# Kernel tuning notes

Hardware: AMD Instinct MI355X
Metric: run time of the kernel (lower is better)

## Reference

```python
import jax, jax.numpy as jnp
import numpy as np

NS, NW, E, DIN, OUT, H = 100_000, 400_000, 500_000, 64, 64, 4


def setup_inputs() -> dict:
    key = jax.random.key(0)
    ks = jax.random.split(key, 26)
    s = 1.0 / np.sqrt(DIN)
    sg = 1.0 / np.sqrt(OUT)
    inp = {
        "x_sites": jax.random.normal(ks[0], (NS, DIN), jnp.float32),
        "x_wells": jax.random.normal(ks[1], (NW, DIN), jnp.float32),
        "edge_sw_src": jax.random.randint(ks[2], (E,), 0, NS, jnp.int32),
        "edge_sw_dst": jax.random.randint(ks[3], (E,), 0, NW, jnp.int32),
        "edge_ws_src": jax.random.randint(ks[4], (E,), 0, NW, jnp.int32),
        "edge_ws_dst": jax.random.randint(ks[5], (E,), 0, NS, jnp.int32),
        # GAT ('pfas_sites','distance','gw_wells'), heads=4, concat=False
        "W_sw": jax.random.normal(ks[6], (DIN, H * OUT), jnp.float32) * s,
        "att_src_sw": jax.random.normal(ks[7], (H, OUT), jnp.float32) * sg,
        "att_dst_sw": jax.random.normal(ks[8], (H, OUT), jnp.float32) * sg,
        "b_sw": jnp.zeros((OUT,), jnp.float32),
        # SAGE ('gw_wells','distance','pfas_sites')
        "Wl_ws": jax.random.normal(ks[9], (DIN, OUT), jnp.float32) * s,
        "bl_ws": jnp.zeros((OUT,), jnp.float32),
        "Wr_ws": jax.random.normal(ks[10], (DIN, OUT), jnp.float32) * s,
        # GAT ('pfas_sites','self_loop','pfas_sites'), add_self_loops=True -> identity edges
        "W_ss": jax.random.normal(ks[11], (DIN, H * OUT), jnp.float32) * s,
        "att_src_ss": jax.random.normal(ks[12], (H, OUT), jnp.float32) * sg,
        "att_dst_ss": jax.random.normal(ks[13], (H, OUT), jnp.float32) * sg,
        "b_ss": jnp.zeros((OUT,), jnp.float32),
        # SAGE ('gw_wells','self_loop','gw_wells') with identity edges
        "Wl_ww": jax.random.normal(ks[14], (DIN, OUT), jnp.float32) * s,
        "bl_ww": jnp.zeros((OUT,), jnp.float32),
        "Wr_ww": jax.random.normal(ks[15], (DIN, OUT), jnp.float32) * s,
        # output heads
        "Wg": jax.random.normal(ks[16], (OUT, 1), jnp.float32) * sg,
        "bg": jnp.zeros((1,), jnp.float32),
        "Wsit": jax.random.normal(ks[17], (OUT, 1), jnp.float32) * sg,
        "bsit": jnp.zeros((1,), jnp.float32),
    }
    return inp


def _gat(x_src, x_dst, src, dst, W, a_src, a_dst, b, n_dst):
    """PyG GATConv, concat=False (mean over heads), negative_slope=0.2."""
    h, c = a_src.shape
    xs = (x_src @ W).reshape(-1, h, c)  # [Ns,H,C]
    xd = (x_dst @ W).reshape(-1, h, c)  # [Nd,H,C]
    al_s = jnp.einsum("nhc,hc->nh", xs, a_src)
    al_d = jnp.einsum("nhc,hc->nh", xd, a_dst)
    e = jax.nn.leaky_relu(al_s[src] + al_d[dst], 0.2)  # [E,H]
    m = jax.ops.segment_max(e, dst, num_segments=n_dst)
    ex = jnp.exp(e - m[dst])
    denom = jax.ops.segment_sum(ex, dst, num_segments=n_dst)
    alpha = ex / denom[dst]  # edge-softmax per dst node
    msg = xs[src] * alpha[:, :, None]  # [E,H,C] dominant intermediate
    out = jax.ops.segment_sum(msg, dst, num_segments=n_dst)
    return out.mean(axis=1) + b


def _sage(x_src, x_dst, src, dst, Wl, bl, Wr, n_dst):
    """PyG SAGEConv, mean aggregation, root_weight=True."""
    ssum = jax.ops.segment_sum(x_src[src], dst, num_segments=n_dst)
    cnt = jax.ops.segment_sum(jnp.ones((src.shape[0],), x_src.dtype), dst, num_segments=n_dst)
    mean = ssum / jnp.maximum(cnt, 1.0)[:, None]  # empty neighborhood -> 0 (PyG mean scatter)
    return mean @ Wl + bl + x_dst @ Wr


def reference(x_sites, x_wells, edge_sw_src, edge_sw_dst, edge_ws_src, edge_ws_dst,
              W_sw, att_src_sw, att_dst_sw, b_sw, Wl_ws, bl_ws, Wr_ws,
              W_ss, att_src_ss, att_dst_ss, b_ss, Wl_ww, bl_ww, Wr_ww,
              Wg, bg, Wsit, bsit):
    # relation 1: GAT sites -> wells
    gw = _gat(x_sites, x_wells, edge_sw_src, edge_sw_dst, W_sw, att_src_sw, att_dst_sw, b_sw, NW)
    # relation 4: SAGE self-loop on wells; identity edges -> mean == x itself
    gw = gw + (x_wells @ Wl_ww + bl_ww + x_wells @ Wr_ww)  # HeteroConv aggr='sum'
    # relation 2: SAGE wells -> sites
    si = _sage(x_wells, x_sites, edge_ws_src, edge_ws_dst, Wl_ws, bl_ws, Wr_ws, NS)
    # relation 3: GAT self-loop on sites (add_self_loops=True -> identity edge set);
    # softmax over a single self edge is 1, so output = mean over heads of lin(x) + bias
    si = si + (x_sites @ W_ss).reshape(NS, H, OUT).mean(axis=1) + b_ss
    # post: relu -> dropout (eval mode: identity) -> linear -> leaky_relu(0.01)
    gw = jax.nn.relu(gw)
    si = jax.nn.relu(si)
    o_gw = jax.nn.leaky_relu(gw @ Wg + bg, 0.01)   # [NW, 1]
    o_si = jax.nn.leaky_relu(si @ Wsit + bsit, 0.01)  # [NS, 1]
    return o_gw, o_si
```

## Files before the change

kernel.cpp:

```cpp
#include <hip/hip_runtime.h>

#define NS_ 100000
#define NW_ 400000
#define NE_ 500000
#define EPB 2048

#define SP_BLKS  ((NS_ + 63) / 64)
#define HG_BLKS  ((NE_ + 255) / 256)
#define SAGE_BLKS (NS_ / 16)
#define GAT_BLKS  (NW_ / 16)

typedef float f32x4_t __attribute__((ext_vector_type(4)));
typedef unsigned u32x4_t __attribute__((ext_vector_type(4)));

__device__ __forceinline__ float lrelu02(float x) { return x > 0.f ? x : 0.2f * x; }
__device__ __forceinline__ float bf2f(unsigned short u) {
    return __uint_as_float(((unsigned)u) << 16);
}
__device__ __forceinline__ unsigned short f2bf(float f) {
    unsigned u = __float_as_uint(f);
    u += 0x7FFFu + ((u >> 16) & 1u);
    return (unsigned short)(u >> 16);
}
__device__ __forceinline__ unsigned pk(float lo, float hi) {
    return (unsigned)f2bf(lo) | ((unsigned)f2bf(hi) << 16);
}
__device__ __forceinline__ void mfma_bf16(f32x4_t& acc, u32x4_t a, u32x4_t b) {
    asm volatile("v_mfma_f32_16x16x32_bf16 %0, %1, %2, %0" : "+v"(acc) : "v"(a), "v"(b));
}

__global__ void __launch_bounds__(256)
k_prep(const float* __restrict__ W_sw, const float* __restrict__ att_src,
       const float* __restrict__ att_dst,
       const float* __restrict__ Wl_ww, const float* __restrict__ Wr_ww,
       const float* __restrict__ Wl_ws, const float* __restrict__ Wr_ws,
       const float* __restrict__ W_ss,
       float* __restrict__ vd, float* __restrict__ vs,
       u32x4_t* __restrict__ fw, u32x4_t* __restrict__ fs,
       u32x4_t* __restrict__ fsp)
{
    const int tid = threadIdx.x;
    {
        int d = tid >> 2, h = tid & 3;
        const float4* wp = (const float4*)(W_sw + d * 256 + h * 64);
        const float4* ad = (const float4*)(att_dst + h * 64);
        const float4* as = (const float4*)(att_src + h * 64);
        float accd = 0.f, accs = 0.f;
#pragma unroll
        for (int c = 0; c < 16; ++c) {
            float4 wv = wp[c]; float4 dv = ad[c]; float4 sv = as[c];
            accd += wv.x * dv.x + wv.y * dv.y + wv.z * dv.z + wv.w * dv.w;
            accs += wv.x * sv.x + wv.y * sv.y + wv.z * sv.z + wv.w * sv.w;
        }
        vd[d * 4 + h] = accd;
        vs[d * 4 + h] = accs;
    }
    for (int idx = tid; idx < 512; idx += 256) {
        int f = idx >> 6, lane = idx & 63;
        int kc = f >> 2, ct = f & 3, q = lane >> 4, n = lane & 15;
        int c = ct * 16 + n;
        u32x4_t d;
#pragma unroll
        for (int i = 0; i < 4; ++i) {
            int k = kc * 32 + q * 8 + 2 * i;
            d[i] = pk(Wl_ww[k * 64 + c] + Wr_ww[k * 64 + c],
                      Wl_ww[(k + 1) * 64 + c] + Wr_ww[(k + 1) * 64 + c]);
        }
        fw[idx] = d;
    }
    for (int idx = tid; idx < 1024; idx += 256) {
        int f = idx >> 6, lane = idx & 63;
        int kc = f >> 2, ct = f & 3, q = lane >> 4, n = lane & 15;
        int c = ct * 16 + n;
        u32x4_t d;
#pragma unroll
        for (int i = 0; i < 4; ++i) {
            int k = kc * 32 + q * 8 + 2 * i;
            float lo, hi;
            if (k < 64) {
                lo = Wl_ws[k * 64 + c];
                hi = Wl_ws[(k + 1) * 64 + c];
            } else {
                int kk = k - 64;
                lo = Wr_ws[kk * 64 + c] + 0.25f * (W_ss[kk * 256 + c] + W_ss[kk * 256 + 64 + c] +
                                                   W_ss[kk * 256 + 128 + c] + W_ss[kk * 256 + 192 + c]);
                hi = Wr_ws[(kk + 1) * 64 + c] + 0.25f * (W_ss[(kk + 1) * 256 + c] + W_ss[(kk + 1) * 256 + 64 + c] +
                                                         W_ss[(kk + 1) * 256 + 128 + c] + W_ss[(kk + 1) * 256 + 192 + c]);
            }
            d[i] = pk(lo, hi);
        }
        fs[idx] = d;
    }
    for (int idx = tid; idx < 2048; idx += 256) {
        int f = idx >> 6, lane = idx & 63;
        int kc = f >> 4, ct = f & 15, q = lane >> 4, n = lane & 15;
        int c = ct * 16 + n;
        u32x4_t d;
#pragma unroll
        for (int i = 0; i < 4; ++i) {
            int k = kc * 32 + q * 8 + 2 * i;
            d[i] = pk(W_sw[k * 256 + c], W_sw[(k + 1) * 256 + c]);
        }
        fsp[idx] = d;
    }
}

#define SP_PAD 264
__global__ void __launch_bounds__(256)
k_main1(const float* __restrict__ x_sites, const u32x4_t* __restrict__ fsp,
        const float* __restrict__ vs, unsigned short* __restrict__ xs,
        float* __restrict__ al_s,
        const int* __restrict__ d1, int* __restrict__ h1,
        const int* __restrict__ d2, int* __restrict__ h2)
{
    __shared__ float smem1[8704];
    const int tid = threadIdx.x;
    const int bid = blockIdx.x;
    if (bid >= SP_BLKS) {
        int hb = bid - SP_BLKS;
        int rel = hb / HG_BLKS;
        int e = (hb % HG_BLKS) * 256 + tid;
        if (e < NE_) {
            if (rel == 0) atomicAdd(&h1[d1[e]], 1);
            else          atomicAdd(&h2[d2[e]], 1);
        }
        return;
    }
    unsigned short* stg = (unsigned short*)smem1;
    float* vsl = smem1 + 8448 / 2 * 0 + 8448;
    vsl = smem1 + 8448;
    vsl[tid] = vs[tid];
    __syncthreads();
    const int wave = __builtin_amdgcn_readfirstlane(tid >> 6);
    const int lane = tid & 63, q = lane >> 4, n = lane & 15;
    const int sbase = bid * 64 + wave * 16;
    const int srow = min(sbase + n, NS_ - 1);
    const float* xr = x_sites + (size_t)srow * 64 + q * 8;
    float4 x0 = *(const float4*)(xr);
    float4 x1 = *(const float4*)(xr + 4);
    float4 x2 = *(const float4*)(xr + 32);
    float4 x3 = *(const float4*)(xr + 36);
    u32x4_t am0 = { pk(x0.x, x0.y), pk(x0.z, x0.w), pk(x1.x, x1.y), pk(x1.z, x1.w) };
    u32x4_t am1 = { pk(x2.x, x2.y), pk(x2.z, x2.w), pk(x3.x, x3.y), pk(x3.z, x3.w) };
    float pa[4];
#pragma unroll
    for (int h = 0; h < 4; ++h) {
        const float* v0 = &vsl[(q * 8) * 4 + h];
        const float* v1 = &vsl[(32 + q * 8) * 4 + h];
        pa[h] = x0.x * v0[0]  + x0.y * v0[4]  + x0.z * v0[8]  + x0.w * v0[12]
              + x1.x * v0[16] + x1.y * v0[20] + x1.z * v0[24] + x1.w * v0[28]
              + x2.x * v1[0]  + x2.y * v1[4]  + x2.z * v1[8]  + x2.w * v1[12]
              + x3.x * v1[16] + x3.y * v1[20] + x3.z * v1[24] + x3.w * v1[28];
    }
#pragma unroll
    for (int h = 0; h < 4; ++h) {
        pa[h] += __shfl_xor(pa[h], 16, 64);
        pa[h] += __shfl_xor(pa[h], 32, 64);
    }
    if (q == 0 && sbase + n < NS_)
        *(float4*)(al_s + (size_t)(sbase + n) * 4) = make_float4(pa[0], pa[1], pa[2], pa[3]);

    f32x4_t acc[16];
#pragma unroll
    for (int ct = 0; ct < 16; ++ct) acc[ct] = (f32x4_t){0, 0, 0, 0};
    asm volatile("s_nop 3" : "+v"(am0), "+v"(am1));
#pragma unroll
    for (int ct = 0; ct < 16; ++ct) mfma_bf16(acc[ct], am0, fsp[ct * 64 + lane]);
#pragma unroll
    for (int ct = 0; ct < 16; ++ct) mfma_bf16(acc[ct], am1, fsp[(16 + ct) * 64 + lane]);
    asm volatile("s_nop 7\n\ts_nop 7" ::: "memory");
    unsigned short* ss = stg + wave * (16 * SP_PAD);
#pragma unroll
    for (int ct = 0; ct < 16; ++ct)
#pragma unroll
        for (int reg = 0; reg < 4; ++reg)
            ss[(q * 4 + reg) * SP_PAD + ct * 16 + n] = f2bf(acc[ct][reg]);
    __builtin_amdgcn_s_waitcnt(0);
#pragma unroll
    for (int i = 0; i < 8; ++i) {
        int g = i * 64 + lane;
        int r = g >> 5, c = g & 31;
        if (sbase + r < NS_) {
            u32x4_t v = *(const u32x4_t*)(ss + r * SP_PAD + c * 8);
            *(u32x4_t*)(xs + (size_t)(sbase + r) * 256 + c * 8) = v;
        }
    }
}

__global__ void __launch_bounds__(256)
k_scan1_2(const int* __restrict__ h1, int n1, int* __restrict__ b1, int nb1,
          const int* __restrict__ h2, int n2, int* __restrict__ b2)
{
    __shared__ int red[256];
    const int tid = threadIdx.x;
    const int bx = blockIdx.x;
    const int* hist; int n; int* bsum; int blk;
    if (bx < nb1) { hist = h1; n = n1; bsum = b1; blk = bx; }
    else          { hist = h2; n = n2; bsum = b2; blk = bx - nb1; }
    int base = blk * EPB + tid * 8;
    int s = 0;
#pragma unroll
    for (int i = 0; i < 8; ++i) { int idx = base + i; if (idx < n) s += hist[idx]; }
    red[tid] = s;
    __syncthreads();
    for (int off = 128; off > 0; off >>= 1) {
        if (tid < off) red[tid] += red[tid + off];
        __syncthreads();
    }
    if (tid == 0) bsum[blk] = red[0];
}

__global__ void __launch_bounds__(256)
k_scan2_2(int* __restrict__ b1, int nb1, int* __restrict__ b2, int nb2)
{
    __shared__ int sh[256];
    const int tid = threadIdx.x;
    int* bsum = blockIdx.x == 0 ? b1 : b2;
    int nb = blockIdx.x == 0 ? nb1 : nb2;
    sh[tid] = (tid < nb) ? bsum[tid] : 0;
    __syncthreads();
    for (int off = 1; off < 256; off <<= 1) {
        int u = (tid >= off) ? sh[tid - off] : 0;
        __syncthreads();
        sh[tid] += u;
        __syncthreads();
    }
    if (tid < nb) bsum[tid] = (tid == 0) ? 0 : sh[tid - 1];
}

__global__ void __launch_bounds__(256)
k_scan3_2(const int* __restrict__ h1, int n1, const int* __restrict__ b1,
          int* __restrict__ rp1, int* __restrict__ cu1, int nb1,
          const int* __restrict__ h2, int n2, const int* __restrict__ b2,
          int* __restrict__ rp2, int* __restrict__ cu2)
{
    __shared__ int tsum[256];
    const int tid = threadIdx.x;
    const int bx = blockIdx.x;
    const int* hist; int n; const int* bsum; int* rowptr; int* cursor; int blk;
    if (bx < nb1) { hist = h1; n = n1; bsum = b1; rowptr = rp1; cursor = cu1; blk = bx; }
    else          { hist = h2; n = n2; bsum = b2; rowptr = rp2; cursor = cu2; blk = bx - nb1; }
    int base = blk * EPB + tid * 8;
    int v[8]; int s = 0;
#pragma unroll
    for (int i = 0; i < 8; ++i) {
        int idx = base + i;
        v[i] = (idx < n) ? hist[idx] : 0;
        s += v[i];
    }
    tsum[tid] = s;
    __syncthreads();
    for (int off = 1; off < 256; off <<= 1) {
        int u = (tid >= off) ? tsum[tid - off] : 0;
        __syncthreads();
        tsum[tid] += u;
        __syncthreads();
    }
    int texcl = tsum[tid] - s;
    int run = bsum[blk] + texcl;
#pragma unroll
    for (int i = 0; i < 8; ++i) {
        int idx = base + i;
        if (idx < n) { rowptr[idx] = run; cursor[idx] = run; run += v[i]; }
    }
    if (blk == 0 && tid == 0) rowptr[n] = NE_;
}

__global__ void __launch_bounds__(256)
k_scatter2(const int* __restrict__ s1, const int* __restrict__ d1,
           int* __restrict__ c1, int* __restrict__ o1,
           const int* __restrict__ s2, const int* __restrict__ d2,
           int* __restrict__ c2, int* __restrict__ o2)
{
    int e = blockIdx.x * 256 + threadIdx.x;
    if (e >= NE_) return;
    if (blockIdx.y == 0) { int p = atomicAdd(&c1[d1[e]], 1); o1[p] = s1[e]; }
    else                 { int p = atomicAdd(&c2[d2[e]], 1); o2[p] = s2[e]; }
}

__global__ void __launch_bounds__(256)
k_main6(const float* __restrict__ x_sites, const float* __restrict__ x_wells,
        const int* __restrict__ rp_ws, const int* __restrict__ csr_ws,
        const u32x4_t* __restrict__ fs, const float* __restrict__ bl_ws,
        const float* __restrict__ b_ss, const float* __restrict__ Wsit,
        const float* __restrict__ bsit,
        const float* __restrict__ vd, const int* __restrict__ rp_sw,
        const int* __restrict__ csr_sw, const float* __restrict__ al_s,
        const unsigned short* __restrict__ xs, const float* __restrict__ b_sw,
        const float* __restrict__ bl_ww, const u32x4_t* __restrict__ fw,
        const float* __restrict__ Wg, const float* __restrict__ bg,
        float* __restrict__ out)
{
    __shared__ float smem[2400];
    const int tid = threadIdx.x;
    const int bid = blockIdx.x;

    if (bid < SAGE_BLKS) {
        unsigned* mnB = (unsigned*)smem;
        unsigned* xB  = (unsigned*)(smem + 576);
        float* dl     = smem + 1152;
        float* biasl  = smem + 2240;
        float* wsl    = smem + 2304;
        float* res    = smem + 2368;
        if (tid < 64) { biasl[tid] = bl_ws[tid] + b_ss[tid]; wsl[tid] = Wsit[tid]; }
        const int sl = tid >> 4, p = tid & 15;
        const int s = bid * 16 + sl;
        const int r0 = rp_ws[s], r1 = rp_ws[s + 1];
        float4 m4 = {0.f, 0.f, 0.f, 0.f};
        for (int j = r0; j < r1; ++j) {
            int wsrc = csr_ws[j];
            float4 xv = ((const float4*)(x_wells + (size_t)wsrc * 64))[p];
            m4.x += xv.x; m4.y += xv.y; m4.z += xv.z; m4.w += xv.w;
        }
        if (r1 > r0) {
            float rc = 1.f / (float)(r1 - r0);
            m4.x *= rc; m4.y *= rc; m4.z *= rc; m4.w *= rc;
        }
        {
            int c0 = (2 * p + 8 * sl) & 31;
            mnB[sl * 36 + c0]     = pk(m4.x, m4.y);
            mnB[sl * 36 + c0 + 1] = pk(m4.z, m4.w);
            float4 xv = *(const float4*)(x_sites + (size_t)s * 64 + 4 * p);
            xB[sl * 36 + c0]     = pk(xv.x, xv.y);
            xB[sl * 36 + c0 + 1] = pk(xv.z, xv.w);
        }
        __syncthreads();
        const int wave = __builtin_amdgcn_readfirstlane(tid >> 6);
        const int lane = tid & 63, q = lane >> 4, n = lane & 15;
        const int b0 = (4 * q + 8 * n) & 31;
        const int b1 = (16 + 4 * q + 8 * n) & 31;
        u32x4_t am0 = *(const u32x4_t*)&mnB[n * 36 + b0];
        u32x4_t am1 = *(const u32x4_t*)&mnB[n * 36 + b1];
        u32x4_t ax0 = *(const u32x4_t*)&xB[n * 36 + b0];
        u32x4_t ax1 = *(const u32x4_t*)&xB[n * 36 + b1];
        f32x4_t acc = {0, 0, 0, 0};
        asm volatile("s_nop 3" : "+v"(am0), "+v"(am1), "+v"(ax0), "+v"(ax1), "+v"(acc));
        mfma_bf16(acc, am0, fs[wave * 64 + lane]);
        mfma_bf16(acc, am1, fs[(4 + wave) * 64 + lane]);
        mfma_bf16(acc, ax0, fs[(8 + wave) * 64 + lane]);
        mfma_bf16(acc, ax1, fs[(12 + wave) * 64 + lane]);
        asm volatile("s_nop 7\n\ts_nop 7" : "+v"(acc));
#pragma unroll
        for (int reg = 0; reg < 4; ++reg)
            dl[(q * 4 + reg) * 68 + wave * 16 + n] = acc[reg];
        __syncthreads();
        const int c0 = 4 * p;
        float4 dv = *(const float4*)&dl[sl * 68 + c0];
        float t0 = dv.x + biasl[c0];
        float t1 = dv.y + biasl[c0 + 1];
        float t2 = dv.z + biasl[c0 + 2];
        float t3 = dv.w + biasl[c0 + 3];
        float pr = fmaxf(t0, 0.f) * wsl[c0] + fmaxf(t1, 0.f) * wsl[c0 + 1] +
                   fmaxf(t2, 0.f) * wsl[c0 + 2] + fmaxf(t3, 0.f) * wsl[c0 + 3];
        pr += __shfl_xor(pr, 1, 64);
        pr += __shfl_xor(pr, 2, 64);
        pr += __shfl_xor(pr, 4, 64);
        pr += __shfl_xor(pr, 8, 64);
        if (p == 0) res[sl] = pr + bsit[0];
        __syncthreads();
        if (tid < 16) {
            float v = res[tid];
            out[(size_t)NW_ + bid * 16 + tid] = v > 0.f ? v : 0.01f * v;
        }
        return;
    }

    {
        const int gb = bid - SAGE_BLKS;
        float* vdl    = smem;
        unsigned* xwB = (unsigned*)(smem + 272);
        float* dl     = smem + 848;
        float* biasl  = smem + 1936;
        float* wgl    = smem + 2000;
        float* res    = smem + 2064;
        vdl[(tid >> 4) * 17 + (tid & 15)] = vd[tid];
        if (tid < 64) { biasl[tid] = b_sw[tid] + bl_ww[tid]; wgl[tid] = Wg[tid]; }
        __syncthreads();
        const int wl = tid >> 4, p = tid & 15;
        const int w = gb * 16 + wl;
        const int r0 = rp_sw[w], r1 = rp_sw[w + 1];
        float h0, h1, h2, h3;
        {
            float4 xv = *(const float4*)(x_wells + (size_t)w * 64 + 4 * p);
            int c0 = (2 * p + 8 * wl) & 31;
            xwB[wl * 36 + c0]     = pk(xv.x, xv.y);
            xwB[wl * 36 + c0 + 1] = pk(xv.z, xv.w);
            const float* vp = &vdl[p * 17];
            h0 = xv.x * vp[0] + xv.y * vp[4] + xv.z * vp[8]  + xv.w * vp[12];
            h1 = xv.x * vp[1] + xv.y * vp[5] + xv.z * vp[9]  + xv.w * vp[13];
            h2 = xv.x * vp[2] + xv.y * vp[6] + xv.z * vp[10] + xv.w * vp[14];
            h3 = xv.x * vp[3] + xv.y * vp[7] + xv.z * vp[11] + xv.w * vp[15];
        }
#pragma unroll
        for (int off = 1; off < 16; off <<= 1) {
            h0 += __shfl_xor(h0, off, 64);
            h1 += __shfl_xor(h1, off, 64);
            h2 += __shfl_xor(h2, off, 64);
            h3 += __shfl_xor(h3, off, 64);
        }
        float den0 = 0, den1 = 0, den2 = 0, den3 = 0;
        float n0[4] = {0, 0, 0, 0}, n1[4] = {0, 0, 0, 0};
        float n2[4] = {0, 0, 0, 0}, n3[4] = {0, 0, 0, 0};
        for (int j = r0; j < r1; ++j) {
            int s = csr_sw[j];
            float4 as = ((const float4*)al_s)[s];
            float e0 = __expf(lrelu02(as.x + h0));
            float e1 = __expf(lrelu02(as.y + h1));
            float e2 = __expf(lrelu02(as.z + h2));
            float e3 = __expf(lrelu02(as.w + h3));
            den0 += e0; den1 += e1; den2 += e2; den3 += e3;
            const unsigned short* xr = xs + (size_t)s * 256 + 4 * p;
            ushort4 u0 = *(const ushort4*)(xr);
            ushort4 u1 = *(const ushort4*)(xr + 64);
            ushort4 u2 = *(const ushort4*)(xr + 128);
            ushort4 u3 = *(const ushort4*)(xr + 192);
            n0[0] += e0 * bf2f(u0.x); n0[1] += e0 * bf2f(u0.y); n0[2] += e0 * bf2f(u0.z); n0[3] += e0 * bf2f(u0.w);
            n1[0] += e1 * bf2f(u1.x); n1[1] += e1 * bf2f(u1.y); n1[2] += e1 * bf2f(u1.z); n1[3] += e1 * bf2f(u1.w);
            n2[0] += e2 * bf2f(u2.x); n2[1] += e2 * bf2f(u2.y); n2[2] += e2 * bf2f(u2.z); n2[3] += e2 * bf2f(u2.w);
            n3[0] += e3 * bf2f(u3.x); n3[1] += e3 * bf2f(u3.y); n3[2] += e3 * bf2f(u3.z); n3[3] += e3 * bf2f(u3.w);
        }
        const int c0 = 4 * p;
        float tmsg[4];
        if (r1 > r0) {
            float i0 = 0.25f / den0, i1 = 0.25f / den1, i2 = 0.25f / den2, i3 = 0.25f / den3;
#pragma unroll
            for (int i = 0; i < 4; ++i)
                tmsg[i] = n0[i] * i0 + n1[i] * i1 + n2[i] * i2 + n3[i] * i3 + biasl[c0 + i];
        } else {
#pragma unroll
            for (int i = 0; i < 4; ++i) tmsg[i] = biasl[c0 + i];
        }
        __syncthreads();
        const int wave = __builtin_amdgcn_readfirstlane(tid >> 6);
        const int lane = tid & 63, q = lane >> 4, n = lane & 15;
        const int b0 = (4 * q + 8 * n) & 31;
        const int b1 = (16 + 4 * q + 8 * n) & 31;
        u32x4_t ax0 = *(const u32x4_t*)&xwB[n * 36 + b0];
        u32x4_t ax1 = *(const u32x4_t*)&xwB[n * 36 + b1];
        f32x4_t acc = {0, 0, 0, 0};
        asm volatile("s_nop 3" : "+v"(ax0), "+v"(ax1), "+v"(acc));
        mfma_bf16(acc, ax0, fw[wave * 64 + lane]);
        mfma_bf16(acc, ax1, fw[(4 + wave) * 64 + lane]);
        asm volatile("s_nop 7\n\ts_nop 7" : "+v"(acc));
#pragma unroll
        for (int reg = 0; reg < 4; ++reg)
            dl[(q * 4 + reg) * 68 + wave * 16 + n] = acc[reg];
        __syncthreads();
        float4 dv = *(const float4*)&dl[wl * 68 + c0];
        float t0 = tmsg[0] + dv.x;
        float t1 = tmsg[1] + dv.y;
        float t2 = tmsg[2] + dv.z;
        float t3 = tmsg[3] + dv.w;
        float pr = fmaxf(t0, 0.f) * wgl[c0] + fmaxf(t1, 0.f) * wgl[c0 + 1] +
                   fmaxf(t2, 0.f) * wgl[c0 + 2] + fmaxf(t3, 0.f) * wgl[c0 + 3];
        pr += __shfl_xor(pr, 1, 64);
        pr += __shfl_xor(pr, 2, 64);
        pr += __shfl_xor(pr, 4, 64);
        pr += __shfl_xor(pr, 8, 64);
        if (p == 0) res[wl] = pr + bg[0];
        __syncthreads();
        if (tid < 16) {
            float v = res[tid];
            out[gb * 16 + tid] = v > 0.f ? v : 0.01f * v;
        }
    }
}

extern "C" void kernel_launch(void* const* d_in, const int* in_sizes, int n_in,
                              void* d_out, int out_size, void* d_ws, size_t ws_size,
                              hipStream_t stream)
{
    const float* x_sites    = (const float*)d_in[0];
    const float* x_wells    = (const float*)d_in[1];
    const int*   e_sw_src   = (const int*)d_in[2];
    const int*   e_sw_dst   = (const int*)d_in[3];
    const int*   e_ws_src   = (const int*)d_in[4];
    const int*   e_ws_dst   = (const int*)d_in[5];
    const float* W_sw       = (const float*)d_in[6];
    const float* att_src_sw = (const float*)d_in[7];
    const float* att_dst_sw = (const float*)d_in[8];
    const float* b_sw       = (const float*)d_in[9];
    const float* Wl_ws      = (const float*)d_in[10];
    const float* bl_ws      = (const float*)d_in[11];
    const float* Wr_ws      = (const float*)d_in[12];
    const float* W_ss       = (const float*)d_in[13];
    const float* b_ss       = (const float*)d_in[16];
    const float* Wl_ww      = (const float*)d_in[17];
    const float* bl_ww      = (const float*)d_in[18];
    const float* Wr_ww      = (const float*)d_in[19];
    const float* Wg         = (const float*)d_in[20];
    const float* bg         = (const float*)d_in[21];
    const float* Wsit       = (const float*)d_in[22];
    const float* bsit       = (const float*)d_in[23];
    float* out = (float*)d_out;

    unsigned short* xs = (unsigned short*)d_ws;
    float* al_s = (float*)(xs + (size_t)NS_ * 256);
    float* vd   = al_s + (size_t)NS_ * 4;
    float* vs   = vd + 256;
    u32x4_t* fw = (u32x4_t*)(vs + 256);
    u32x4_t* fs = fw + 512;
    u32x4_t* fsp= fs + 1024;
    int* ip     = (int*)(fsp + 2048);
    int* h_sw   = ip;
    int* h_ws   = h_sw + NW_;
    int* rp_sw  = h_ws + NS_;
    int* cur_sw = rp_sw + NW_ + 4;
    int* csr_sw = cur_sw + NW_;
    int* bs_sw  = csr_sw + NE_;
    int* rp_ws  = bs_sw + 256;
    int* cur_ws = rp_ws + NS_ + 4;
    int* csr_ws = cur_ws + NS_;
    int* bs_ws  = csr_ws + NE_;

    hipMemsetAsync(h_sw, 0, (size_t)(NW_ + NS_) * sizeof(int), stream);

    const int egrid = HG_BLKS;
    const int nb_sw = (NW_ + EPB - 1) / EPB;
    const int nb_ws = (NS_ + EPB - 1) / EPB;

    hipLaunchKernelGGL(k_prep, dim3(1), dim3(256), 0, stream,
                       W_sw, att_src_sw, att_dst_sw, Wl_ww, Wr_ww, Wl_ws, Wr_ws, W_ss,
                       vd, vs, fw, fs, fsp);

    hipLaunchKernelGGL(k_main1, dim3(SP_BLKS + 2 * HG_BLKS), dim3(256), 0, stream,
                       x_sites, fsp, vs, xs, al_s,
                       e_sw_dst, h_sw, e_ws_dst, h_ws);

    hipLaunchKernelGGL(k_scan1_2, dim3(nb_sw + nb_ws), dim3(256), 0, stream,
                       h_sw, NW_, bs_sw, nb_sw, h_ws, NS_, bs_ws);
    hipLaunchKernelGGL(k_scan2_2, dim3(2), dim3(256), 0, stream,
                       bs_sw, nb_sw, bs_ws, nb_ws);
    hipLaunchKernelGGL(k_scan3_2, dim3(nb_sw + nb_ws), dim3(256), 0, stream,
                       h_sw, NW_, bs_sw, rp_sw, cur_sw, nb_sw,
                       h_ws, NS_, bs_ws, rp_ws, cur_ws);
    hipLaunchKernelGGL(k_scatter2, dim3(egrid, 2), dim3(256), 0, stream,
                       e_sw_src, e_sw_dst, cur_sw, csr_sw,
                       e_ws_src, e_ws_dst, cur_ws, csr_ws);

    hipLaunchKernelGGL(k_main6, dim3(SAGE_BLKS + GAT_BLKS), dim3(256), 0, stream,
                       x_sites, x_wells, rp_ws, csr_ws, fs, bl_ws, b_ss, Wsit, bsit,
                       vd, rp_sw, csr_sw, al_s, xs, b_sw, bl_ww, fw, Wg, bg, out);
}
```

Measured before the change: 481.8 us.

## Split site preprocessing from histogram, parallelize prep, and reorganize bf16 layout for gather

Several changes land at once. The weight-prep kernel now spreads its work over 15 blocks instead of one. The site projection moves out of the histogram kernel into its own launch just before the final kernel, and the SAGE and GAT blocks in the final kernel are interleaved 1:4. The xs bf16 layout is permuted so each GAT edge gather reads two contiguous 16-byte vectors instead of four 8-byte ones, the LDS XOR swizzles are dropped, and nontemporal loads are added for the x rows. The aim is less serial prep time, fewer and wider gather transactions, better load balance, and keeping the xs table hot in cache right before its consumer. The cost is an extra kernel launch and possible LDS bank conflicts now that the swizzle is gone.

New measurement: 470.8 us. 1.02x faster.

```diff
diff --git a/kernel.cpp b/kernel.cpp
--- a/kernel.cpp
+++ b/kernel.cpp
@@ -5,8 +5,6 @@
 #define NE_ 500000
 #define EPB 2048
 
-#define SP_BLKS  ((NS_ + 63) / 64)
-#define HG_BLKS  ((NE_ + 255) / 256)
 #define SAGE_BLKS (NS_ / 16)
 #define GAT_BLKS  (NW_ / 16)
 
@@ -17,6 +15,8 @@
 __device__ __forceinline__ float bf2f(unsigned short u) {
     return __uint_as_float(((unsigned)u) << 16);
 }
+__device__ __forceinline__ float lo16(unsigned u) { return __uint_as_float(u << 16); }
+__device__ __forceinline__ float hi16(unsigned u) { return __uint_as_float(u & 0xFFFF0000u); }
 __device__ __forceinline__ unsigned short f2bf(float f) {
     unsigned u = __float_as_uint(f);
     u += 0x7FFFu + ((u >> 16) & 1u);
@@ -40,7 +40,8 @@
        u32x4_t* __restrict__ fsp)
 {
     const int tid = threadIdx.x;
-    {
+    const int bid = blockIdx.x;
+    if (bid == 0) {
         int d = tid >> 2, h = tid & 3;
         const float4* wp = (const float4*)(W_sw + d * 256 + h * 64);
         const float4* ad = (const float4*)(att_dst + h * 64);
@@ -54,8 +55,8 @@
         }
         vd[d * 4 + h] = accd;
         vs[d * 4 + h] = accs;
-    }
-    for (int idx = tid; idx < 512; idx += 256) {
+    } else if (bid <= 2) {
+        int idx = (bid - 1) * 256 + tid;
         int f = idx >> 6, lane = idx & 63;
         int kc = f >> 2, ct = f & 3, q = lane >> 4, n = lane & 15;
         int c = ct * 16 + n;
@@ -67,8 +68,8 @@
                       Wl_ww[(k + 1) * 64 + c] + Wr_ww[(k + 1) * 64 + c]);
         }
         fw[idx] = d;
-    }
-    for (int idx = tid; idx < 1024; idx += 256) {
+    } else if (bid <= 6) {
+        int idx = (bid - 3) * 256 + tid;
         int f = idx >> 6, lane = idx & 63;
         int kc = f >> 2, ct = f & 3, q = lane >> 4, n = lane & 15;
         int c = ct * 16 + n;
@@ -90,8 +91,8 @@
             d[i] = pk(lo, hi);
         }
         fs[idx] = d;
-    }
-    for (int idx = tid; idx < 2048; idx += 256) {
+    } else {
+        int idx = (bid - 7) * 256 + tid;
         int f = idx >> 6, lane = idx & 63;
         int kc = f >> 4, ct = f & 15, q = lane >> 4, n = lane & 15;
         int c = ct * 16 + n;
@@ -107,50 +108,35 @@
 
 #define SP_PAD 264
 __global__ void __launch_bounds__(256)
-k_main1(const float* __restrict__ x_sites, const u32x4_t* __restrict__ fsp,
-        const float* __restrict__ vs, unsigned short* __restrict__ xs,
-        float* __restrict__ al_s,
-        const int* __restrict__ d1, int* __restrict__ h1,
-        const int* __restrict__ d2, int* __restrict__ h2)
-{
-    __shared__ float smem1[8704];
+k_sites_pre(const float* __restrict__ x_sites, const u32x4_t* __restrict__ fsp,
+            const float* __restrict__ vs, unsigned short* __restrict__ xs,
+            float* __restrict__ al_s)
+{
+    __shared__ unsigned short stg[4][16 * SP_PAD];
+    __shared__ float vsl[256];
     const int tid = threadIdx.x;
-    const int bid = blockIdx.x;
-    if (bid >= SP_BLKS) {
-        int hb = bid - SP_BLKS;
-        int rel = hb / HG_BLKS;
-        int e = (hb % HG_BLKS) * 256 + tid;
-        if (e < NE_) {
-            if (rel == 0) atomicAdd(&h1[d1[e]], 1);
-            else          atomicAdd(&h2[d2[e]], 1);
-        }
-        return;
-    }
-    unsigned short* stg = (unsigned short*)smem1;
-    float* vsl = smem1 + 8448 / 2 * 0 + 8448;
-    vsl = smem1 + 8448;
     vsl[tid] = vs[tid];
     __syncthreads();
     const int wave = __builtin_amdgcn_readfirstlane(tid >> 6);
     const int lane = tid & 63, q = lane >> 4, n = lane & 15;
-    const int sbase = bid * 64 + wave * 16;
+    const int sbase = blockIdx.x * 64 + wave * 16;
     const int srow = min(sbase + n, NS_ - 1);
     const float* xr = x_sites + (size_t)srow * 64 + q * 8;
-    float4 x0 = *(const float4*)(xr);
-    float4 x1 = *(const float4*)(xr + 4);
-    float4 x2 = *(const float4*)(xr + 32);
-    float4 x3 = *(const float4*)(xr + 36);
-    u32x4_t am0 = { pk(x0.x, x0.y), pk(x0.z, x0.w), pk(x1.x, x1.y), pk(x1.z, x1.w) };
-    u32x4_t am1 = { pk(x2.x, x2.y), pk(x2.z, x2.w), pk(x3.x, x3.y), pk(x3.z, x3.w) };
+    f32x4_t x0 = __builtin_nontemporal_load((const f32x4_t*)(xr));
+    f32x4_t x1 = __builtin_nontemporal_load((const f32x4_t*)(xr + 4));
+    f32x4_t x2 = __builtin_nontemporal_load((const f32x4_t*)(xr + 32));
+    f32x4_t x3 = __builtin_nontemporal_load((const f32x4_t*)(xr + 36));
+    u32x4_t am0 = { pk(x0[0], x0[1]), pk(x0[2], x0[3]), pk(x1[0], x1[1]), pk(x1[2], x1[3]) };
+    u32x4_t am1 = { pk(x2[0], x2[1]), pk(x2[2], x2[3]), pk(x3[0], x3[1]), pk(x3[2], x3[3]) };
     float pa[4];
 #pragma unroll
     for (int h = 0; h < 4; ++h) {
         const float* v0 = &vsl[(q * 8) * 4 + h];
         const float* v1 = &vsl[(32 + q * 8) * 4 + h];
-        pa[h] = x0.x * v0[0]  + x0.y * v0[4]  + x0.z * v0[8]  + x0.w * v0[12]
-              + x1.x * v0[16] + x1.y * v0[20] + x1.z * v0[24] + x1.w * v0[28]
-              + x2.x * v1[0]  + x2.y * v1[4]  + x2.z * v1[8]  + x2.w * v1[12]
-              + x3.x * v1[16] + x3.y * v1[20] + x3.z * v1[24] + x3.w * v1[28];
+        pa[h] = x0[0] * v0[0]  + x0[1] * v0[4]  + x0[2] * v0[8]  + x0[3] * v0[12]
+              + x1[0] * v0[16] + x1[1] * v0[20] + x1[2] * v0[24] + x1[3] * v0[28]
+              + x2[0] * v1[0]  + x2[1] * v1[4]  + x2[2] * v1[8]  + x2[3] * v1[12]
+              + x3[0] * v1[16] + x3[1] * v1[20] + x3[2] * v1[24] + x3[3] * v1[28];
     }
 #pragma unroll
     for (int h = 0; h < 4; ++h) {
@@ -169,12 +155,15 @@
 #pragma unroll
     for (int ct = 0; ct < 16; ++ct) mfma_bf16(acc[ct], am1, fsp[(16 + ct) * 64 + lane]);
     asm volatile("s_nop 7\n\ts_nop 7" ::: "memory");
-    unsigned short* ss = stg + wave * (16 * SP_PAD);
-#pragma unroll
-    for (int ct = 0; ct < 16; ++ct)
+    unsigned short* ss = &stg[wave][0];
+    const int pbase = ((n >> 2) * 16) + (n & 3);
+#pragma unroll
+    for (int ct = 0; ct < 16; ++ct) {
+        const int cidx = pbase + (ct & 3) * 64 + (ct >> 2) * 4;
 #pragma unroll
         for (int reg = 0; reg < 4; ++reg)
-            ss[(q * 4 + reg) * SP_PAD + ct * 16 + n] = f2bf(acc[ct][reg]);
+            ss[(q * 4 + reg) * SP_PAD + cidx] = f2bf(acc[ct][reg]);
+    }
     __builtin_amdgcn_s_waitcnt(0);
 #pragma unroll
     for (int i = 0; i < 8; ++i) {
@@ -185,6 +174,16 @@
             *(u32x4_t*)(xs + (size_t)(sbase + r) * 256 + c * 8) = v;
         }
     }
+}
+
+__global__ void __launch_bounds__(256)
+k_hist2(const int* __restrict__ d1, int* __restrict__ h1,
+        const int* __restrict__ d2, int* __restrict__ h2)
+{
+    int e = blockIdx.x * 256 + threadIdx.x;
+    if (e >= NE_) return;
+    if (blockIdx.y == 0) atomicAdd(&h1[d1[e]], 1);
+    else                 atomicAdd(&h2[d2[e]], 1);
 }
 
 __global__ void __launch_bounds__(256)
@@ -279,23 +278,24 @@
 }
 
 __global__ void __launch_bounds__(256)
-k_main6(const float* __restrict__ x_sites, const float* __restrict__ x_wells,
-        const int* __restrict__ rp_ws, const int* __restrict__ csr_ws,
-        const u32x4_t* __restrict__ fs, const float* __restrict__ bl_ws,
-        const float* __restrict__ b_ss, const float* __restrict__ Wsit,
-        const float* __restrict__ bsit,
-        const float* __restrict__ vd, const int* __restrict__ rp_sw,
-        const int* __restrict__ csr_sw, const float* __restrict__ al_s,
-        const unsigned short* __restrict__ xs, const float* __restrict__ b_sw,
-        const float* __restrict__ bl_ww, const u32x4_t* __restrict__ fw,
-        const float* __restrict__ Wg, const float* __restrict__ bg,
-        float* __restrict__ out)
-{
-    __shared__ float smem[2400];
+k_fin(const float* __restrict__ x_sites, const float* __restrict__ x_wells,
+      const int* __restrict__ rp_ws, const int* __restrict__ csr_ws,
+      const u32x4_t* __restrict__ fs, const float* __restrict__ bl_ws,
+      const float* __restrict__ b_ss, const float* __restrict__ Wsit,
+      const float* __restrict__ bsit,
+      const float* __restrict__ vd, const int* __restrict__ rp_sw,
+      const int* __restrict__ csr_sw, const float* __restrict__ al_s,
+      const unsigned short* __restrict__ xs, const float* __restrict__ b_sw,
+      const float* __restrict__ bl_ww, const u32x4_t* __restrict__ fw,
+      const float* __restrict__ Wg, const float* __restrict__ bg,
+      float* __restrict__ out)
+{
+    __shared__ float smem[2384];
     const int tid = threadIdx.x;
     const int bid = blockIdx.x;
 
-    if (bid < SAGE_BLKS) {
+    if (bid % 5 == 0) {
+        const int sb = bid / 5;
         unsigned* mnB = (unsigned*)smem;
         unsigned* xB  = (unsigned*)(smem + 576);
         float* dl     = smem + 1152;
@@ -304,7 +304,7 @@
         float* res    = smem + 2368;
         if (tid < 64) { biasl[tid] = bl_ws[tid] + b_ss[tid]; wsl[tid] = Wsit[tid]; }
         const int sl = tid >> 4, p = tid & 15;
-        const int s = bid * 16 + sl;
+        const int s = sb * 16 + sl;
         const int r0 = rp_ws[s], r1 = rp_ws[s + 1];
         float4 m4 = {0.f, 0.f, 0.f, 0.f};
         for (int j = r0; j < r1; ++j) {
@@ -316,23 +316,21 @@
             float rc = 1.f / (float)(r1 - r0);
             m4.x *= rc; m4.y *= rc; m4.z *= rc; m4.w *= rc;
         }
+        mnB[sl * 36 + 2 * p]     = pk(m4.x, m4.y);
+        mnB[sl * 36 + 2 * p + 1] = pk(m4.z, m4.w);
         {
-            int c0 = (2 * p + 8 * sl) & 31;
-            mnB[sl * 36 + c0]     = pk(m4.x, m4.y);
-            mnB[sl * 36 + c0 + 1] = pk(m4.z, m4.w);
-            float4 xv = *(const float4*)(x_sites + (size_t)s * 64 + 4 * p);
-            xB[sl * 36 + c0]     = pk(xv.x, xv.y);
-            xB[sl * 36 + c0 + 1] = pk(xv.z, xv.w);
+            f32x4_t xv = __builtin_nontemporal_load(
+                (const f32x4_t*)(x_sites + (size_t)s * 64 + 4 * p));
+            xB[sl * 36 + 2 * p]     = pk(xv[0], xv[1]);
+            xB[sl * 36 + 2 * p + 1] = pk(xv[2], xv[3]);
         }
         __syncthreads();
         const int wave = __builtin_amdgcn_readfirstlane(tid >> 6);
         const int lane = tid & 63, q = lane >> 4, n = lane & 15;
-        const int b0 = (4 * q + 8 * n) & 31;
-        const int b1 = (16 + 4 * q + 8 * n) & 31;
-        u32x4_t am0 = *(const u32x4_t*)&mnB[n * 36 + b0];
-        u32x4_t am1 = *(const u32x4_t*)&mnB[n * 36 + b1];
-        u32x4_t ax0 = *(const u32x4_t*)&xB[n * 36 + b0];
-        u32x4_t ax1 = *(const u32x4_t*)&xB[n * 36 + b1];
+        u32x4_t am0 = *(const u32x4_t*)&mnB[n * 36 + q * 4];
+        u32x4_t am1 = *(const u32x4_t*)&mnB[n * 36 + 16 + q * 4];
+        u32x4_t ax0 = *(const u32x4_t*)&xB[n * 36 + q * 4];
+        u32x4_t ax1 = *(const u32x4_t*)&xB[n * 36 + 16 + q * 4];
         f32x4_t acc = {0, 0, 0, 0};
         asm volatile("s_nop 3" : "+v"(am0), "+v"(am1), "+v"(ax0), "+v"(ax1), "+v"(acc));
         mfma_bf16(acc, am0, fs[wave * 64 + lane]);
@@ -360,13 +358,13 @@
         __syncthreads();
         if (tid < 16) {
             float v = res[tid];
-            out[(size_t)NW_ + bid * 16 + tid] = v > 0.f ? v : 0.01f * v;
+            out[(size_t)NW_ + sb * 16 + tid] = v > 0.f ? v : 0.01f * v;
         }
         return;
     }
 
     {
-        const int gb = bid - SAGE_BLKS;
+        const int gb = bid - 1 - bid / 5;
         float* vdl    = smem;
         unsigned* xwB = (unsigned*)(smem + 272);
         float* dl     = smem + 848;
@@ -381,15 +379,15 @@
         const int r0 = rp_sw[w], r1 = rp_sw[w + 1];
         float h0, h1, h2, h3;
         {
-            float4 xv = *(const float4*)(x_wells + (size_t)w * 64 + 4 * p);
-            int c0 = (2 * p + 8 * wl) & 31;
-            xwB[wl * 36 + c0]     = pk(xv.x, xv.y);
-            xwB[wl * 36 + c0 + 1] = pk(xv.z, xv.w);
+            f32x4_t xv = __builtin_nontemporal_load(
+                (const f32x4_t*)(x_wells + (size_t)w * 64 + 4 * p));
+            xwB[wl * 36 + 2 * p]     = pk(xv[0], xv[1]);
+            xwB[wl * 36 + 2 * p + 1] = pk(xv[2], xv[3]);
             const float* vp = &vdl[p * 17];
-            h0 = xv.x * vp[0] + xv.y * vp[4] + xv.z * vp[8]  + xv.w * vp[12];
-            h1 = xv.x * vp[1] + xv.y * vp[5] + xv.z * vp[9]  + xv.w * vp[13];
-            h2 = xv.x * vp[2] + xv.y * vp[6] + xv.z * vp[10] + xv.w * vp[14];
-            h3 = xv.x * vp[3] + xv.y * vp[7] + xv.z * vp[11] + xv.w * vp[15];
+            h0 = xv[0] * vp[0] + xv[1] * vp[4] + xv[2] * vp[8]  + xv[3] * vp[12];
+            h1 = xv[0] * vp[1] + xv[1] * vp[5] + xv[2] * vp[9]  + xv[3] * vp[13];
+            h2 = xv[0] * vp[2] + xv[1] * vp[6] + xv[2] * vp[10] + xv[3] * vp[14];
+            h3 = xv[0] * vp[3] + xv[1] * vp[7] + xv[2] * vp[11] + xv[3] * vp[15];
         }
 #pragma unroll
         for (int off = 1; off < 16; off <<= 1) {
@@ -404,20 +402,22 @@
         for (int j = r0; j < r1; ++j) {
             int s = csr_sw[j];
             float4 as = ((const float4*)al_s)[s];
+            const unsigned short* xr = xs + (size_t)s * 256 + p * 16;
+            u32x4_t va = *(const u32x4_t*)(xr);
+            u32x4_t vb = *(const u32x4_t*)(xr + 8);
             float e0 = __expf(lrelu02(as.x + h0));
             float e1 = __expf(lrelu02(as.y + h1));
             float e2 = __expf(lrelu02(as.z + h2));
             float e3 = __expf(lrelu02(as.w + h3));
             den0 += e0; den1 += e1; den2 += e2; den3 += e3;
-            const unsigned short* xr = xs + (size_t)s * 256 + 4 * p;
-            ushort4 u0 = *(const ushort4*)(xr);
-            ushort4 u1 = *(const ushort4*)(xr + 64);
-            ushort4 u2 = *(const ushort4*)(xr + 128);
-            ushort4 u3 = *(const ushort4*)(xr + 192);
-            n0[0] += e0 * bf2f(u0.x); n0[1] += e0 * bf2f(u0.y); n0[2] += e0 * bf2f(u0.z); n0[3] += e0 * bf2f(u0.w);
-            n1[0] += e1 * bf2f(u1.x); n1[1] += e1 * bf2f(u1.y); n1[2] += e1 * bf2f(u1.z); n1[3] += e1 * bf2f(u1.w);
-            n2[0] += e2 * bf2f(u2.x); n2[1] += e2 * bf2f(u2.y); n2[2] += e2 * bf2f(u2.z); n2[3] += e2 * bf2f(u2.w);
-            n3[0] += e3 * bf2f(u3.x); n3[1] += e3 * bf2f(u3.y); n3[2] += e3 * bf2f(u3.z); n3[3] += e3 * bf2f(u3.w);
+            n0[0] += e0 * lo16(va[0]); n0[1] += e0 * hi16(va[0]);
+            n0[2] += e0 * lo16(va[1]); n0[3] += e0 * hi16(va[1]);
+            n1[0] += e1 * lo16(va[2]); n1[1] += e1 * hi16(va[2]);
+            n1[2] += e1 * lo16(va[3]); n1[3] += e1 * hi16(va[3]);
+            n2[0] += e2 * lo16(vb[0]); n2[1] += e2 * hi16(vb[0]);
+            n2[2] += e2 * lo16(vb[1]); n2[3] += e2 * hi16(vb[1]);
+            n3[0] += e3 * lo16(vb[2]); n3[1] += e3 * hi16(vb[2]);
+            n3[2] += e3 * lo16(vb[3]); n3[3] += e3 * hi16(vb[3]);
         }
         const int c0 = 4 * p;
         float tmsg[4];
@@ -433,10 +433,8 @@
         __syncthreads();
         const int wave = __builtin_amdgcn_readfirstlane(tid >> 6);
         const int lane = tid & 63, q = lane >> 4, n = lane & 15;
-        const int b0 = (4 * q + 8 * n) & 31;
-        const int b1 = (16 + 4 * q + 8 * n) & 31;
-        u32x4_t ax0 = *(const u32x4_t*)&xwB[n * 36 + b0];
-        u32x4_t ax1 = *(const u32x4_t*)&xwB[n * 36 + b1];
+        u32x4_t ax0 = *(const u32x4_t*)&xwB[n * 36 + q * 4];
+        u32x4_t ax1 = *(const u32x4_t*)&xwB[n * 36 + 16 + q * 4];
         f32x4_t acc = {0, 0, 0, 0};
         asm volatile("s_nop 3" : "+v"(ax0), "+v"(ax1), "+v"(acc));
         mfma_bf16(acc, ax0, fw[wave * 64 + lane]);
@@ -515,18 +513,16 @@
 
     hipMemsetAsync(h_sw, 0, (size_t)(NW_ + NS_) * sizeof(int), stream);
 
-    const int egrid = HG_BLKS;
+    const int egrid = (NE_ + 255) / 256;
     const int nb_sw = (NW_ + EPB - 1) / EPB;
     const int nb_ws = (NS_ + EPB - 1) / EPB;
 
-    hipLaunchKernelGGL(k_prep, dim3(1), dim3(256), 0, stream,
+    hipLaunchKernelGGL(k_prep, dim3(15), dim3(256), 0, stream,
                        W_sw, att_src_sw, att_dst_sw, Wl_ww, Wr_ww, Wl_ws, Wr_ws, W_ss,
                        vd, vs, fw, fs, fsp);
 
-    hipLaunchKernelGGL(k_main1, dim3(SP_BLKS + 2 * HG_BLKS), dim3(256), 0, stream,
-                       x_sites, fsp, vs, xs, al_s,
+    hipLaunchKernelGGL(k_hist2, dim3(egrid, 2), dim3(256), 0, stream,
                        e_sw_dst, h_sw, e_ws_dst, h_ws);
-
     hipLaunchKernelGGL(k_scan1_2, dim3(nb_sw + nb_ws), dim3(256), 0, stream,
                        h_sw, NW_, bs_sw, nb_sw, h_ws, NS_, bs_ws);
     hipLaunchKernelGGL(k_scan2_2, dim3(2), dim3(256), 0, stream,
@@ -538,7 +534,10 @@
                        e_sw_src, e_sw_dst, cur_sw, csr_sw,
                        e_ws_src, e_ws_dst, cur_ws, csr_ws);
 
-    hipLaunchKernelGGL(k_main6, dim3(SAGE_BLKS + GAT_BLKS), dim3(256), 0, stream,
+    hipLaunchKernelGGL(k_sites_pre, dim3((NS_ + 63) / 64), dim3(256), 0, stream,
+                       x_sites, fsp, vs, xs, al_s);
+
+    hipLaunchKernelGGL(k_fin, dim3(SAGE_BLKS + GAT_BLKS), dim3(256), 0, stream,
                        x_sites, x_wells, rp_ws, csr_ws, fs, bl_ws, b_ss, Wsit, bsit,
                        vd, rp_sw, csr_sw, al_s, xs, b_sw, bl_ww, fw, Wg, bg, out);
 }
```
